# Kernel tuning notes

Measured on AMD Instinct MI355X. Metric: run time of the kernel, lower is better.

Reference implementation:

```python
import jax, jax.numpy as jnp
import numpy as np

N = 100000        # nodes
E = 1600000       # edges (before self-loops)
IN = 128          # in_dim
HID = 16          # hidden_dim per head
HEADS = 8
OUT = 40          # out_dim (classes)
BN_EPS = 1e-5
NEG_SLOPE = 0.2


def setup_inputs() -> dict:
    key = jax.random.key(0)
    ks = jax.random.split(key, 16)
    s = 0.05
    return {
        "x": jax.random.normal(ks[0], (N, IN), dtype=jnp.float32),
        "edge_index": jax.random.randint(ks[1], (2, E), 0, N, dtype=jnp.int64),
        "W1": jax.random.normal(ks[2], (IN, HEADS * HID), dtype=jnp.float32) * s,
        "att_src1": jax.random.normal(ks[3], (HEADS, HID), dtype=jnp.float32) * s,
        "att_dst1": jax.random.normal(ks[4], (HEADS, HID), dtype=jnp.float32) * s,
        "bias1": jax.random.normal(ks[5], (HEADS * HID,), dtype=jnp.float32) * s,
        "bn_gamma": 1.0 + jax.random.normal(ks[6], (HEADS * HID,), dtype=jnp.float32) * 0.1,
        "bn_beta": jax.random.normal(ks[7], (HEADS * HID,), dtype=jnp.float32) * 0.1,
        "bn_mean": jax.random.normal(ks[8], (HEADS * HID,), dtype=jnp.float32) * 0.1,
        "bn_var": jax.random.uniform(ks[9], (HEADS * HID,), dtype=jnp.float32, minval=0.5, maxval=1.5),
        "W2": jax.random.normal(ks[10], (HEADS * HID, OUT), dtype=jnp.float32) * s,
        "att_src2": jax.random.normal(ks[11], (1, OUT), dtype=jnp.float32) * s,
        "att_dst2": jax.random.normal(ks[12], (1, OUT), dtype=jnp.float32) * s,
        "bias2": jax.random.normal(ks[13], (OUT,), dtype=jnp.float32) * s,
        "W_skip": jax.random.normal(ks[14], (IN, HEADS * HID), dtype=jnp.float32) * s,
        "b_skip": jax.random.normal(ks[15], (HEADS * HID,), dtype=jnp.float32) * s,
    }


def gat_conv(x, src, dst, W, a_src, a_dst, bias, heads, ch, concat):
    """PyG GATConv (eval mode): per-edge attention, segment softmax over dst, scatter-add."""
    n = x.shape[0]
    h = (x @ W).reshape(n, heads, ch)                      # [N,H,C]
    alpha_s = jnp.einsum("nhc,hc->nh", h, a_src)            # [N,H]
    alpha_d = jnp.einsum("nhc,hc->nh", h, a_dst)            # [N,H]
    e = jax.nn.leaky_relu(alpha_s[src] + alpha_d[dst], NEG_SLOPE)   # [E,H]
    # numerically stable segment softmax over destination node
    m = jax.ops.segment_max(e, dst, num_segments=n)          # [N,H]
    ex = jnp.exp(e - m[dst])                                 # [E,H]
    denom = jax.ops.segment_sum(ex, dst, num_segments=n)     # [N,H]
    alpha = ex / (denom[dst] + 1e-16)                        # [E,H]
    out = jax.ops.segment_sum(alpha[:, :, None] * h[src], dst, num_segments=n)  # [N,H,C]
    out = out.reshape(n, heads * ch) if concat else out.mean(axis=1)
    return out + bias


def reference(x, edge_index, W1, att_src1, att_dst1, bias1,
              bn_gamma, bn_beta, bn_mean, bn_var,
              W2, att_src2, att_dst2, bias2, W_skip, b_skip):
    n = x.shape[0]
    # add self-loops (PyG GATConv default)
    loops = jnp.arange(n, dtype=edge_index.dtype)
    src = jnp.concatenate([edge_index[0], loops])
    dst = jnp.concatenate([edge_index[1], loops])

    identity = x @ W_skip + b_skip                           # skip projection

    h = gat_conv(x, src, dst, W1, att_src1, att_dst1, bias1, HEADS, HID, True)
    h = (h - bn_mean) * (bn_gamma / jnp.sqrt(bn_var + BN_EPS)) + bn_beta  # BN eval
    h = jax.nn.elu(h)                                        # dropout: eval no-op
    h = h + identity

    att_s2 = att_src2  # [1,OUT] heads=1
    out = gat_conv(h, src, dst, W2, att_s2, att_dst2, bias2, 1, OUT, False)
    return jax.nn.log_softmax(out, axis=1)
```

## Files before the change

kernel.cpp:

```cpp
#include <hip/hip_runtime.h>
#include <math.h>

#define NEG_SLOPE 0.2f
#define BN_EPS 1e-5f
#define BSH 9
#define BMASK 511
#define LOG2E 1.44269504088896f
#define BCAP 12288

typedef __attribute__((ext_vector_type(8))) short short8;
typedef __attribute__((ext_vector_type(4))) float f32x4;

__device__ __forceinline__ float wave_max64(float v) {
  #pragma unroll
  for (int o = 32; o; o >>= 1) v = fmaxf(v, __shfl_xor(v, o, 64));
  return v;
}
__device__ __forceinline__ float wave_sum64(float v) {
  #pragma unroll
  for (int o = 32; o; o >>= 1) v += __shfl_xor(v, o, 64);
  return v;
}

__device__ __forceinline__ unsigned pack2bf(float a, float b) {
  unsigned ua = __float_as_uint(a);
  unsigned ub = __float_as_uint(b);
  ua = ua + 0x7fffu + ((ua >> 16) & 1u);
  ub = ub + 0x7fffu + ((ub >> 16) & 1u);
  return (ua >> 16) | (ub & 0xffff0000u);
}
__device__ __forceinline__ float bf_lo(unsigned u) { return __uint_as_float(u << 16); }
__device__ __forceinline__ float bf_hi(unsigned u) { return __uint_as_float(u & 0xffff0000u); }

union U8 { short8 s; uint4 u; };

__global__ void prep_kernel(const float* __restrict__ W1,
                            const float* __restrict__ att_s,
                            const float* __restrict__ att_d,
                            float* __restrict__ Mext,
                            const float* __restrict__ W2,
                            const float* __restrict__ att_s2,
                            const float* __restrict__ att_d2,
                            float* __restrict__ M2ext)
{
  int k = threadIdx.x;
  #pragma unroll
  for (int h = 0; h < 8; ++h) {
    float s = 0.f, d = 0.f;
    #pragma unroll
    for (int c = 0; c < 16; ++c) {
      float w = W1[k * 128 + h * 16 + c];
      s += w * att_s[h * 16 + c];
      d += w * att_d[h * 16 + c];
    }
    Mext[k * 16 + h] = s * LOG2E;
    Mext[k * 16 + 8 + h] = d * LOG2E;
  }
  float s2 = 0.f, d2 = 0.f;
  #pragma unroll
  for (int c = 0; c < 40; ++c) {
    float w = W2[k * 40 + c];
    s2 += w * att_s2[c];
    d2 += w * att_d2[c];
  }
  M2ext[k * 2] = s2 * LOG2E;
  M2ext[k * 2 + 1] = d2 * LOG2E;
}

__global__ __launch_bounds__(256) void gemm1_scatter_kernel(
    const float* __restrict__ X, const float* __restrict__ W1,
    const float* __restrict__ Wsk, const float* __restrict__ bsk,
    const float* __restrict__ Mext,
    unsigned short* __restrict__ h1f8, unsigned* __restrict__ identb,
    float* __restrict__ alpha_s, float* __restrict__ alpha_d, int N,
    const int* __restrict__ esrc, const int* __restrict__ edst,
    int* __restrict__ bcur, unsigned* __restrict__ pkbuf,
    int E, int T, int chunk, int NB, int G1)
{
  __shared__ uint4 Asm4[2048];
  const int t = threadIdx.x;

  if ((int)blockIdx.x >= G1) {
    int* hist  = (int*)Asm4;
    int* lbase = hist + 256;
    int* lcur  = hist + 512;
    const int bid = (int)blockIdx.x - G1;
    hist[t] = 0;
    __syncthreads();
    int s0 = bid * chunk;
    int s1 = min(s0 + chunk, T);
    for (int i = s0 + t; i < s1; i += 256) {
      int d = (i < E) ? edst[i] : (i - E);
      atomicAdd(&hist[d >> BSH], 1);
    }
    __syncthreads();
    if (t < NB) {
      int h = hist[t];
      lbase[t] = t * BCAP + (h ? atomicAdd(&bcur[t], h) : 0);
      lcur[t] = 0;
    }
    __syncthreads();
    for (int i = s0 + t; i < s1; i += 256) {
      int d, s;
      if (i < E) { d = edst[i]; s = esrc[i]; } else { d = s = i - E; }
      int b = d >> BSH;
      int p = lbase[b] + atomicAdd(&lcur[b], 1);
      pkbuf[p] = ((unsigned)(d & BMASK) << 17) | (unsigned)s;
    }
    return;
  }

  const int l = t & 63, wave = t >> 6;
  const int lx = l & 15, ly = l >> 4;
  const int row0 = blockIdx.x * 128;
  const int wn0 = wave * 64;

  short8 b[4][4];
  short8 b4[4] = {};
  #pragma unroll
  for (int nf = 0; nf < 4; ++nf) {
    int c = wn0 + nf * 16 + lx;
    const float* bp = (c < 128) ? (W1 + c) : (Wsk + c - 128);
    #pragma unroll
    for (int kf = 0; kf < 4; ++kf) {
      int k0 = kf * 32 + ly * 8;
      U8 f;
      f.u.x = pack2bf(bp[(k0 + 0) * 128], bp[(k0 + 1) * 128]);
      f.u.y = pack2bf(bp[(k0 + 2) * 128], bp[(k0 + 3) * 128]);
      f.u.z = pack2bf(bp[(k0 + 4) * 128], bp[(k0 + 5) * 128]);
      f.u.w = pack2bf(bp[(k0 + 6) * 128], bp[(k0 + 7) * 128]);
      b[nf][kf] = f.s;
    }
  }
  if (wave == 0) {
    const float* bp = Mext + lx;
    #pragma unroll
    for (int kf = 0; kf < 4; ++kf) {
      int k0 = kf * 32 + ly * 8;
      U8 f;
      f.u.x = pack2bf(bp[(k0 + 0) * 16], bp[(k0 + 1) * 16]);
      f.u.y = pack2bf(bp[(k0 + 2) * 16], bp[(k0 + 3) * 16]);
      f.u.z = pack2bf(bp[(k0 + 4) * 16], bp[(k0 + 5) * 16]);
      f.u.w = pack2bf(bp[(k0 + 6) * 16], bp[(k0 + 7) * 16]);
      b4[kf] = f.s;
    }
  }

  {
    int rl = t >> 1;
    int half = t & 1;
    int r = row0 + rl;
    const float* xp = X + (size_t)r * 128 + half * 64;
    #pragma unroll
    for (int i = 0; i < 8; ++i) {
      float4 f0 = make_float4(0.f, 0.f, 0.f, 0.f), f1 = f0;
      if (r < N) {
        f0 = *(const float4*)(xp + i * 8);
        f1 = *(const float4*)(xp + i * 8 + 4);
      }
      uint4 u;
      u.x = pack2bf(f0.x, f0.y); u.y = pack2bf(f0.z, f0.w);
      u.z = pack2bf(f1.x, f1.y); u.w = pack2bf(f1.z, f1.w);
      int woff = (rl * 256 + half * 128 + i * 16) ^ ((rl & 7) << 4);
      *(uint4*)((char*)Asm4 + woff) = u;
    }
  }
  __syncthreads();

  float bval[4];
  if (wave >= 2) {
    #pragma unroll
    for (int nf = 0; nf < 4; ++nf) bval[nf] = bsk[(wave - 2) * 64 + nf * 16 + lx];
  }

  for (int mf = 0; mf < 8; ++mf) {
    short8 a[4];
    int rowl = mf * 16 + lx;
    #pragma unroll
    for (int kf = 0; kf < 4; ++kf)
      a[kf] = *(short8*)((char*)Asm4 + ((rowl * 256 + kf * 64 + ly * 16) ^ ((lx & 7) << 4)));

    int rbase = row0 + mf * 16 + ly * 4;

    #pragma unroll
    for (int nf = 0; nf < 4; ++nf) {
      f32x4 acc = {0.f, 0.f, 0.f, 0.f};
      #pragma unroll
      for (int kf = 0; kf < 4; ++kf)
        acc = __builtin_amdgcn_mfma_f32_16x16x32_bf16(a[kf], b[nf][kf], acc, 0, 0, 0);
      if (wave < 2) {
        int c = wn0 + nf * 16 + lx;
        #pragma unroll
        for (int reg = 0; reg < 4; ++reg) {
          float v = acc[reg];
          float vp = __shfl_xor(v, 1, 64);
          int r = rbase + reg;
          if (!(lx & 1) && r < N) {
            int u = __builtin_amdgcn_cvt_pk_fp8_f32(v, vp, 0, false);
            *(unsigned short*)((char*)h1f8 + (unsigned)r * 128u + (unsigned)c) =
                (unsigned short)u;
          }
        }
      } else {
        int c = (wave - 2) * 64 + nf * 16 + lx;
        #pragma unroll
        for (int reg = 0; reg < 4; ++reg) {
          float v = acc[reg] + bval[nf];
          float vp = __shfl_xor(v, 1, 64);
          int r = rbase + reg;
          if (!(lx & 1) && r < N)
            identb[(unsigned)r * 64u + (unsigned)(c >> 1)] = pack2bf(v, vp);
        }
      }
    }

    if (wave == 0) {
      f32x4 acc = {0.f, 0.f, 0.f, 0.f};
      #pragma unroll
      for (int kf = 0; kf < 4; ++kf)
        acc = __builtin_amdgcn_mfma_f32_16x16x32_bf16(a[kf], b4[kf], acc, 0, 0, 0);
      #pragma unroll
      for (int reg = 0; reg < 4; ++reg) {
        int r = rbase + reg;
        if (r < N) {
          if (lx < 8) alpha_s[(size_t)r * 8 + lx] = acc[reg];
          else        alpha_d[(size_t)r * 8 + (lx - 8)] = acc[reg];
        }
      }
    }
  }
}

__global__ __launch_bounds__(256) void passB_kernel(
    const unsigned* __restrict__ pkbuf, const int* __restrict__ bcnt,
    int* __restrict__ starts, int* __restrict__ ends,
    int* __restrict__ ssrc, int N)
{
  __shared__ int cnt[512];
  __shared__ int ps[256];
  __shared__ int cur[512];
  const int t = threadIdx.x;
  const int b = blockIdx.x;
  const int bs = b * BCAP;
  const int be = bs + bcnt[b];

  cnt[t] = 0; cnt[t + 256] = 0;
  __syncthreads();
  for (int i = bs + t; i < be; i += 256)
    atomicAdd(&cnt[pkbuf[i] >> 17], 1);
  __syncthreads();

  int a = cnt[2 * t], b2 = cnt[2 * t + 1];
  ps[t] = a + b2;
  __syncthreads();
  for (int d = 1; d < 256; d <<= 1) {
    int u = (t >= d) ? ps[t - d] : 0;
    __syncthreads();
    ps[t] += u;
    __syncthreads();
  }
  int excl = ps[t] - (a + b2);
  cur[2 * t] = excl;
  cur[2 * t + 1] = excl + a;
  __syncthreads();

  const int node0 = b << BSH;
  {
    int n0 = node0 + 2 * t, n1 = node0 + 2 * t + 1;
    if (n0 < N) { starts[n0] = bs + cur[2 * t];     ends[n0] = bs + cur[2 * t] + a; }
    if (n1 < N) { starts[n1] = bs + cur[2 * t + 1]; ends[n1] = bs + cur[2 * t + 1] + b2; }
  }
  __syncthreads();

  for (int i = bs + t; i < be; i += 256) {
    unsigned pk = pkbuf[i];
    int d = pk >> 17;
    int p = atomicAdd(&cur[d], 1);
    ssrc[bs + p] = (int)(pk & 0x1FFFFu);
  }
}

__global__ __launch_bounds__(256) void agg1_kernel(
    const int* __restrict__ starts, const int* __restrict__ ends,
    const int* __restrict__ ssrc,
    const float* __restrict__ as1, const float* __restrict__ ad1,
    const unsigned short* __restrict__ h1f8,
    const float* __restrict__ bias1, const float* __restrict__ gamma,
    const float* __restrict__ beta, const float* __restrict__ mean,
    const float* __restrict__ var,
    const unsigned* __restrict__ identb, unsigned* __restrict__ hpostb, int N)
{
  const int w = threadIdx.x >> 6, l = threadIdx.x & 63;
  const int n = blockIdx.x * 4 + w;
  if (n >= N) return;
  const int e8 = l >> 3;
  const int hh = l & 7;
  const int h2_4 = (l >> 3) * 4;
  const int c0 = l * 2;
  const unsigned l2 = (unsigned)(l * 2);
  const float adp = ad1[(unsigned)n * 8u + (unsigned)hh];
  const int jb = starts[n], je = ends[n];

  const float bb0 = bias1[c0], bb1 = bias1[c0 + 1];
  const float sc0 = gamma[c0] * rsqrtf(var[c0] + BN_EPS);
  const float sc1 = gamma[c0 + 1] * rsqrtf(var[c0 + 1] + BN_EPS);
  const float mn0 = mean[c0], mn1 = mean[c0 + 1];
  const float bt0 = beta[c0], bt1 = beta[c0 + 1];

  const char* h1c = (const char*)h1f8;

  float dsum = 0.f, a0 = 0.f, a1 = 0.f;

#define PHASE2(K, SVEC, EW) { \
    unsigned sk = (unsigned)__builtin_amdgcn_readlane(SVEC, (K) * 8); \
    float ewk = __uint_as_float( \
        __builtin_amdgcn_ds_bpermute(h2_4 + (K) * 32, __float_as_uint(EW))); \
    unsigned u8 = *(const unsigned short*)(h1c + ((size_t)sk << 7) + l2); \
    a0 += ewk * __builtin_amdgcn_cvt_f32_fp8(u8, 0); \
    a1 += ewk * __builtin_amdgcn_cvt_f32_fp8(u8, 1); }

  int j = jb;
  for (; j + 8 <= je; j += 8) {
    int svec = ssrc[j + e8];
    float e = as1[(unsigned)svec * 8u + (unsigned)hh] + adp;
    e = fmaxf(e, NEG_SLOPE * e);
    float ew = exp2f(e);
    dsum += ew;
    PHASE2(0, svec, ew) PHASE2(1, svec, ew) PHASE2(2, svec, ew) PHASE2(3, svec, ew)
    PHASE2(4, svec, ew) PHASE2(5, svec, ew) PHASE2(6, svec, ew) PHASE2(7, svec, ew)
  }
  int rem = je - j;
  if (rem > 0) {
    int jj = j + (e8 < rem ? e8 : 0);
    int svec = ssrc[jj];
    float e = as1[(unsigned)svec * 8u + (unsigned)hh] + adp;
    e = fmaxf(e, NEG_SLOPE * e);
    float ew = (e8 < rem) ? exp2f(e) : 0.f;
    dsum += ew;
    for (int k = 0; k < rem; ++k) {
      unsigned sk = (unsigned)__builtin_amdgcn_readlane(svec, k * 8);
      float ewk = __uint_as_float(
          __builtin_amdgcn_ds_bpermute(h2_4 + (k << 5), __float_as_uint(ew)));
      unsigned u8 = *(const unsigned short*)(h1c + ((size_t)sk << 7) + l2);
      a0 += ewk * __builtin_amdgcn_cvt_f32_fp8(u8, 0);
      a1 += ewk * __builtin_amdgcn_cvt_f32_fp8(u8, 1);
    }
  }
#undef PHASE2

  dsum += __shfl_xor(dsum, 8, 64);
  dsum += __shfl_xor(dsum, 16, 64);
  dsum += __shfl_xor(dsum, 32, 64);
  float denom = __uint_as_float(
      __builtin_amdgcn_ds_bpermute(h2_4, __float_as_uint(dsum)));

  float inv = 1.f / (denom + 1e-16f);
  unsigned uid = identb[(unsigned)n * 64u + (unsigned)l];
  float o0 = a0 * inv + bb0;
  float o1 = a1 * inv + bb1;
  o0 = (o0 - mn0) * sc0 + bt0;
  o1 = (o1 - mn1) * sc1 + bt1;
  o0 = o0 > 0.f ? o0 : expm1f(o0);
  o1 = o1 > 0.f ? o1 : expm1f(o1);
  o0 += bf_lo(uid); o1 += bf_hi(uid);
  hpostb[(unsigned)n * 64u + (unsigned)l] = pack2bf(o0, o1);
}

__global__ __launch_bounds__(256) void gemm2_kernel(
    const unsigned* __restrict__ hpostb, const float* __restrict__ W2,
    const float* __restrict__ M2ext,
    unsigned* __restrict__ h2a, unsigned* __restrict__ h2b2,
    float* __restrict__ as2, float* __restrict__ ad2, int N)
{
  const int t = threadIdx.x;
  const int l = t & 63, wave = t >> 6;
  const int lx = l & 15, ly = l >> 4;
  const int row0 = blockIdx.x * 128;

  short8 b[3][4];
  short8 b4[4];
  {
    #pragma unroll
    for (int nf = 0; nf < 3; ++nf) {
      int col = nf * 16 + lx;
      bool v = col < 40;
      const float* bp = W2 + (v ? col : 0);
      #pragma unroll
      for (int kf = 0; kf < 4; ++kf) {
        int k0 = kf * 32 + ly * 8;
        U8 f;
        if (v) {
          f.u.x = pack2bf(bp[(k0 + 0) * 40], bp[(k0 + 1) * 40]);
          f.u.y = pack2bf(bp[(k0 + 2) * 40], bp[(k0 + 3) * 40]);
          f.u.z = pack2bf(bp[(k0 + 4) * 40], bp[(k0 + 5) * 40]);
          f.u.w = pack2bf(bp[(k0 + 6) * 40], bp[(k0 + 7) * 40]);
        } else {
          f.u = make_uint4(0, 0, 0, 0);
        }
        b[nf][kf] = f.s;
      }
    }
    bool va = lx < 2;
    const float* bp = M2ext + (va ? lx : 0);
    #pragma unroll
    for (int kf = 0; kf < 4; ++kf) {
      int k0 = kf * 32 + ly * 8;
      U8 f;
      if (va) {
        f.u.x = pack2bf(bp[(k0 + 0) * 2], bp[(k0 + 1) * 2]);
        f.u.y = pack2bf(bp[(k0 + 2) * 2], bp[(k0 + 3) * 2]);
        f.u.z = pack2bf(bp[(k0 + 4) * 2], bp[(k0 + 5) * 2]);
        f.u.w = pack2bf(bp[(k0 + 6) * 2], bp[(k0 + 7) * 2]);
      } else {
        f.u = make_uint4(0, 0, 0, 0);
      }
      b4[kf] = f.s;
    }
  }

  #pragma unroll
  for (int i2 = 0; i2 < 2; ++i2) {
    int mf = wave * 2 + i2;
    int arow = row0 + mf * 16 + lx;
    short8 a[4];
    #pragma unroll
    for (int kf = 0; kf < 4; ++kf) {
      U8 f;
      f.u = make_uint4(0, 0, 0, 0);
      if (arow < N)
        f.u = *(const uint4*)(hpostb + (unsigned)arow * 64u + (unsigned)(kf * 16 + ly * 4));
      a[kf] = f.s;
    }

    int rbase = row0 + mf * 16 + ly * 4;

    #pragma unroll
    for (int nf = 0; nf < 3; ++nf) {
      f32x4 acc = {0.f, 0.f, 0.f, 0.f};
      #pragma unroll
      for (int kf = 0; kf < 4; ++kf)
        acc = __builtin_amdgcn_mfma_f32_16x16x32_bf16(a[kf], b[nf][kf], acc, 0, 0, 0);
      int c = nf * 16 + lx;
      int cp = c >> 1;
      #pragma unroll
      for (int reg = 0; reg < 4; ++reg) {
        float v = acc[reg];
        float vp = __shfl_xor(v, 1, 64);
        int r = rbase + reg;
        if (r < N && c < 40 && !(lx & 1)) {
          unsigned pk = pack2bf(v, vp);
          if (cp < 16) h2a[((unsigned)r << 4) + (unsigned)cp] = pk;
          else         h2b2[((unsigned)r << 2) + (unsigned)(cp - 16)] = pk;
        }
      }
    }
    {
      f32x4 acc = {0.f, 0.f, 0.f, 0.f};
      #pragma unroll
      for (int kf = 0; kf < 4; ++kf)
        acc = __builtin_amdgcn_mfma_f32_16x16x32_bf16(a[kf], b4[kf], acc, 0, 0, 0);
      #pragma unroll
      for (int reg = 0; reg < 4; ++reg) {
        int r = rbase + reg;
        if (r < N) {
          if (lx == 0) as2[r] = acc[reg];
          else if (lx == 1) ad2[r] = acc[reg];
        }
      }
    }
  }
}

__global__ __launch_bounds__(256) void agg2_kernel(
    const int* __restrict__ starts, const int* __restrict__ ends,
    const int* __restrict__ ssrc,
    const float* __restrict__ as2, const float* __restrict__ ad2,
    const unsigned* __restrict__ h2a, const unsigned* __restrict__ h2b2,
    const float* __restrict__ bias2,
    float* __restrict__ outp, int N)
{
  const int w = threadIdx.x >> 6, l = threadIdx.x & 63;
  const int n = blockIdx.x * 4 + w;
  if (n >= N) return;
  const int g = l / 20;
  const int cl = l - g * 20;
  const bool act = l < 60;
  const float ad = ad2[n];
  const int jb = starts[n], je = ends[n];

  const char* hbase = (cl < 16) ? ((const char*)h2a + (unsigned)cl * 4u)
                                : ((const char*)h2b2 + (unsigned)(cl - 16) * 4u);
  const unsigned hshift = (cl < 16) ? 6u : 4u;
  const char* as2c = (const char*)as2;

  float denom = 0.f, a0 = 0.f, a1 = 0.f;

#define EDGE2(JJ, GUARD) { \
    bool v = act && (GUARD); \
    unsigned s = v ? (unsigned)ssrc[JJ] : 0u; \
    float e = *(const float*)(as2c + (s << 2)) + ad; \
    e = fmaxf(e, NEG_SLOPE * e); \
    float ex = v ? exp2f(e) : 0.f; \
    unsigned u = *(const unsigned*)(hbase + ((size_t)s << hshift)); \
    denom += ex; \
    a0 += ex * bf_lo(u); \
    a1 += ex * bf_hi(u); }

  int j = jb;
  for (; j + 9 <= je; j += 9) {
    EDGE2(j + g, true)
    EDGE2(j + 3 + g, true)
    EDGE2(j + 6 + g, true)
  }
  for (; j < je; j += 3) {
    EDGE2(j + g, (j + g) < je)
  }
#undef EDGE2

  a0 += __shfl(a0, l + 20, 64) + __shfl(a0, l + 40, 64);
  a1 += __shfl(a1, l + 20, 64) + __shfl(a1, l + 40, 64);
  denom += __shfl(denom, l + 20, 64) + __shfl(denom, l + 40, 64);

  const int lc = l < 20 ? l : 0;
  float inv = 1.f / (denom + 1e-16f);
  float o0 = a0 * inv + bias2[2 * lc];
  float o1 = a1 * inv + bias2[2 * lc + 1];

  float mx = wave_max64(l < 20 ? fmaxf(o0, o1) : -3.4e38f);
  float se = wave_sum64(l < 20 ? __expf(o0 - mx) + __expf(o1 - mx) : 0.f);
  float ls = logf(se);
  if (l < 20)
    *(float2*)&outp[(size_t)n * 40 + 2 * l] = make_float2(o0 - mx - ls, o1 - mx - ls);
}

extern "C" void kernel_launch(void* const* d_in, const int* in_sizes, int n_in,
                              void* d_out, int out_size, void* d_ws, size_t ws_size,
                              hipStream_t stream)
{
  const float* x        = (const float*)d_in[0];
  const int*   ei       = (const int*)d_in[1];
  const float* W1       = (const float*)d_in[2];
  const float* att_src1 = (const float*)d_in[3];
  const float* att_dst1 = (const float*)d_in[4];
  const float* bias1    = (const float*)d_in[5];
  const float* bn_gamma = (const float*)d_in[6];
  const float* bn_beta  = (const float*)d_in[7];
  const float* bn_mean  = (const float*)d_in[8];
  const float* bn_var   = (const float*)d_in[9];
  const float* W2       = (const float*)d_in[10];
  const float* att_src2 = (const float*)d_in[11];
  const float* att_dst2 = (const float*)d_in[12];
  const float* bias2    = (const float*)d_in[13];
  const float* W_skip   = (const float*)d_in[14];
  const float* b_skip   = (const float*)d_in[15];

  const int N = in_sizes[0] / 128;
  const int E = in_sizes[1] / 2;
  const int T = E + N;
  const int NB = (N + BMASK) >> BSH;

  char* p = (char*)d_ws;
  auto alloc = [&](size_t bytes) { char* q = p; p += (bytes + 255) & ~255ull; return q; };
  unsigned short* h1f8 = (unsigned short*)alloc((size_t)N * 128);
  unsigned* hpostb = (unsigned*)alloc((size_t)N * 64 * 4);
  unsigned* identb = (unsigned*)alloc((size_t)N * 64 * 4);
  float* as1     = (float*)alloc((size_t)N * 8 * 4);
  float* ad1     = (float*)alloc((size_t)N * 8 * 4);
  float* Mext    = (float*)alloc(128 * 16 * 4);
  float* M2ext   = (float*)alloc(128 * 2 * 4);
  int*   starts  = (int*)alloc((size_t)N * 4);
  int*   ends    = (int*)alloc((size_t)N * 4);
  unsigned* pkbuf= (unsigned*)alloc((size_t)NB * BCAP * 4);
  int*   ssrc    = (int*)alloc((size_t)NB * BCAP * 4);
  int*   bcur    = (int*)alloc((size_t)NB * 4);
  unsigned* h2a  = (unsigned*)h1f8;
  unsigned* h2b2 = (unsigned*)((char*)h1f8 + (size_t)N * 64);
  float* as2 = as1;
  float* ad2 = ad1;

  const int* ei_src = ei;
  const int* ei_dst = ei + E;

  hipMemsetAsync(bcur, 0, (size_t)NB * 4, stream);

  prep_kernel<<<1, 128, 0, stream>>>(W1, att_src1, att_dst1, Mext,
                                     W2, att_src2, att_dst2, M2ext);

  const int G1 = (N + 127) / 128;
  const int NBLK_A = 512;
  const int chunk = (T + NBLK_A - 1) / NBLK_A;
  gemm1_scatter_kernel<<<G1 + NBLK_A, 256, 0, stream>>>(
      x, W1, W_skip, b_skip, Mext, h1f8, identb, as1, ad1, N,
      ei_src, ei_dst, bcur, pkbuf, E, T, chunk, NB, G1);

  passB_kernel<<<NB, 256, 0, stream>>>(pkbuf, bcur, starts, ends, ssrc, N);

  agg1_kernel<<<(N + 3) / 4, 256, 0, stream>>>(starts, ends, ssrc, as1, ad1, h1f8,
                                               bias1, bn_gamma, bn_beta, bn_mean, bn_var,
                                               identb, hpostb, N);
  gemm2_kernel<<<(N + 127) / 128, 256, 0, stream>>>(hpostb, W2, M2ext,
                                                    h2a, h2b2, as2, ad2, N);
  agg2_kernel<<<(N + 3) / 4, 256, 0, stream>>>(starts, ends, ssrc, as2, ad2,
                                               h2a, h2b2, bias2,
                                               (float*)d_out, N);
}
```

Baseline: 248.9 us.

## Stage scatter edges in LDS and restructure agg2 with readlane edge broadcast

The scatter blocks now cache each chunk's packed edge word and bucket id in shared memory during the histogram pass, so the second pass no longer re-reads edst/esrc from global memory. The block count is raised if needed so each chunk fits the CH_MAX LDS staging buffer. In agg2, the wave now loads 16 source indices at once, computes their attention weights in parallel, and broadcasts each edge with readlane while the 20 channel lanes accumulate. This replaces the earlier 3-group split and its cross-lane reduction. The change trades redundant global reads and per-lane divergent exp/index loads for more serial per-edge iterations and extra LDS usage.

Measured after the change: 259.7 us. 1.04x slower.

```diff
diff --git a/kernel.cpp b/kernel.cpp
--- a/kernel.cpp
+++ b/kernel.cpp
@@ -7,6 +7,7 @@
 #define BMASK 511
 #define LOG2E 1.44269504088896f
 #define BCAP 12288
+#define CH_MAX 3400
 
 typedef __attribute__((ext_vector_type(8))) short short8;
 typedef __attribute__((ext_vector_type(4))) float f32x4;
@@ -84,14 +85,21 @@
     int* hist  = (int*)Asm4;
     int* lbase = hist + 256;
     int* lcur  = hist + 512;
+    unsigned* spk = (unsigned*)(hist + 768);
+    unsigned char* sbk = (unsigned char*)(spk + CH_MAX);
     const int bid = (int)blockIdx.x - G1;
     hist[t] = 0;
     __syncthreads();
     int s0 = bid * chunk;
     int s1 = min(s0 + chunk, T);
     for (int i = s0 + t; i < s1; i += 256) {
-      int d = (i < E) ? edst[i] : (i - E);
-      atomicAdd(&hist[d >> BSH], 1);
+      int d, s;
+      if (i < E) { d = edst[i]; s = esrc[i]; } else { d = s = i - E; }
+      int b = d >> BSH;
+      int li = i - s0;
+      spk[li] = ((unsigned)(d & BMASK) << 17) | (unsigned)s;
+      sbk[li] = (unsigned char)b;
+      atomicAdd(&hist[b], 1);
     }
     __syncthreads();
     if (t < NB) {
@@ -100,12 +108,11 @@
       lcur[t] = 0;
     }
     __syncthreads();
-    for (int i = s0 + t; i < s1; i += 256) {
-      int d, s;
-      if (i < E) { d = edst[i]; s = esrc[i]; } else { d = s = i - E; }
-      int b = d >> BSH;
+    const int cnt2 = s1 - s0;
+    for (int li = t; li < cnt2; li += 256) {
+      int b = sbk[li];
       int p = lbase[b] + atomicAdd(&lcur[b], 1);
-      pkbuf[p] = ((unsigned)(d & BMASK) << 17) | (unsigned)s;
+      pkbuf[p] = spk[li];
     }
     return;
   }
@@ -482,49 +489,62 @@
   const int w = threadIdx.x >> 6, l = threadIdx.x & 63;
   const int n = blockIdx.x * 4 + w;
   if (n >= N) return;
-  const int g = l / 20;
-  const int cl = l - g * 20;
-  const bool act = l < 60;
+  const int cl = l < 20 ? l : 0;
+  const unsigned ca = (unsigned)((l & 15) * 4);
+  const unsigned cb = (unsigned)((l & 3) * 4);
+  const bool useA = (cl < 16);
   const float ad = ad2[n];
   const int jb = starts[n], je = ends[n];
 
-  const char* hbase = (cl < 16) ? ((const char*)h2a + (unsigned)cl * 4u)
-                                : ((const char*)h2b2 + (unsigned)(cl - 16) * 4u);
-  const unsigned hshift = (cl < 16) ? 6u : 4u;
-  const char* as2c = (const char*)as2;
-
-  float denom = 0.f, a0 = 0.f, a1 = 0.f;
-
-#define EDGE2(JJ, GUARD) { \
-    bool v = act && (GUARD); \
-    unsigned s = v ? (unsigned)ssrc[JJ] : 0u; \
-    float e = *(const float*)(as2c + (s << 2)) + ad; \
-    e = fmaxf(e, NEG_SLOPE * e); \
-    float ex = v ? exp2f(e) : 0.f; \
-    unsigned u = *(const unsigned*)(hbase + ((size_t)s << hshift)); \
-    denom += ex; \
-    a0 += ex * bf_lo(u); \
-    a1 += ex * bf_hi(u); }
+  const char* h2ac = (const char*)h2a;
+  const char* h2bc = (const char*)h2b2;
+
+  float dsum = 0.f, a0 = 0.f, a1 = 0.f;
+
+#define E2PHASE2(K, SVEC, EW) { \
+    unsigned sk = (unsigned)__builtin_amdgcn_readlane(SVEC, (K)); \
+    float ewk = __uint_as_float(__builtin_amdgcn_readlane(__float_as_uint(EW), (K))); \
+    unsigned ua = *(const unsigned*)(h2ac + ((size_t)sk << 6) + ca); \
+    unsigned ub = *(const unsigned*)(h2bc + ((size_t)sk << 4) + cb); \
+    unsigned u = useA ? ua : ub; \
+    a0 += ewk * bf_lo(u); \
+    a1 += ewk * bf_hi(u); }
 
   int j = jb;
-  for (; j + 9 <= je; j += 9) {
-    EDGE2(j + g, true)
-    EDGE2(j + 3 + g, true)
-    EDGE2(j + 6 + g, true)
-  }
-  for (; j < je; j += 3) {
-    EDGE2(j + g, (j + g) < je)
-  }
-#undef EDGE2
-
-  a0 += __shfl(a0, l + 20, 64) + __shfl(a0, l + 40, 64);
-  a1 += __shfl(a1, l + 20, 64) + __shfl(a1, l + 40, 64);
-  denom += __shfl(denom, l + 20, 64) + __shfl(denom, l + 40, 64);
-
-  const int lc = l < 20 ? l : 0;
+  for (; j + 16 <= je; j += 16) {
+    int svec = ssrc[j + (l & 15)];
+    float e = as2[(unsigned)svec] + ad;
+    e = fmaxf(e, NEG_SLOPE * e);
+    float ew = (l < 16) ? exp2f(e) : 0.f;
+    dsum += ew;
+    E2PHASE2(0, svec, ew)  E2PHASE2(1, svec, ew)  E2PHASE2(2, svec, ew)  E2PHASE2(3, svec, ew)
+    E2PHASE2(4, svec, ew)  E2PHASE2(5, svec, ew)  E2PHASE2(6, svec, ew)  E2PHASE2(7, svec, ew)
+    E2PHASE2(8, svec, ew)  E2PHASE2(9, svec, ew)  E2PHASE2(10, svec, ew) E2PHASE2(11, svec, ew)
+    E2PHASE2(12, svec, ew) E2PHASE2(13, svec, ew) E2PHASE2(14, svec, ew) E2PHASE2(15, svec, ew)
+  }
+  int rem = je - j;
+  if (rem > 0) {
+    int svec = ssrc[j + ((l & 15) < rem ? (l & 15) : 0)];
+    float e = as2[(unsigned)svec] + ad;
+    e = fmaxf(e, NEG_SLOPE * e);
+    float ew = (l < rem) ? exp2f(e) : 0.f;
+    dsum += ew;
+    for (int k = 0; k < rem; ++k) {
+      unsigned sk = (unsigned)__builtin_amdgcn_readlane(svec, k);
+      float ewk = __uint_as_float(__builtin_amdgcn_readlane(__float_as_uint(ew), k));
+      unsigned ua = *(const unsigned*)(h2ac + ((size_t)sk << 6) + ca);
+      unsigned ub = *(const unsigned*)(h2bc + ((size_t)sk << 4) + cb);
+      unsigned u = useA ? ua : ub;
+      a0 += ewk * bf_lo(u);
+      a1 += ewk * bf_hi(u);
+    }
+  }
+#undef E2PHASE2
+
+  float denom = wave_sum64(dsum);
   float inv = 1.f / (denom + 1e-16f);
-  float o0 = a0 * inv + bias2[2 * lc];
-  float o1 = a1 * inv + bias2[2 * lc + 1];
+  float o0 = a0 * inv + bias2[2 * cl];
+  float o1 = a1 * inv + bias2[2 * cl + 1];
 
   float mx = wave_max64(l < 20 ? fmaxf(o0, o1) : -3.4e38f);
   float se = wave_sum64(l < 20 ? __expf(o0 - mx) + __expf(o1 - mx) : 0.f);
@@ -587,7 +607,8 @@
                                      W2, att_src2, att_dst2, M2ext);
 
   const int G1 = (N + 127) / 128;
-  const int NBLK_A = 512;
+  int NBLK_A = (T + CH_MAX - 1) / CH_MAX;
+  if (NBLK_A < 512) NBLK_A = 512;
   const int chunk = (T + NBLK_A - 1) / NBLK_A;
   gemm1_scatter_kernel<<<G1 + NBLK_A, 256, 0, stream>>>(
       x, W1, W_skip, b_skip, Mext, h1f8, identb, as1, ad1, N,
```
